# Performance work log

Measured on AMD Instinct MI355X. Metric: run time of the kernel, lower is better.

Reference implementation:

```python
import jax, jax.numpy as jnp
import numpy as np

D_MODEL = 1024
H = 16
DK = 64
DV = 64
D_OUT = 1024
SEQ = 1024
BATCH = 4


def setup_inputs() -> dict:
    key = jax.random.key(0)
    ks = jax.random.split(key, 11)
    s = 0.02
    return {
        "query": jax.random.normal(ks[0], (SEQ, BATCH, D_MODEL), jnp.float32),
        "key": jax.random.normal(ks[1], (SEQ, BATCH, D_MODEL), jnp.float32),
        "value": jax.random.normal(ks[2], (SEQ, BATCH, D_MODEL), jnp.float32),
        "Wq": jax.random.normal(ks[3], (D_MODEL, H * DK), jnp.float32) * s,
        "bq": jnp.zeros((H * DK,), jnp.float32),
        "Wk": jax.random.normal(ks[4], (D_MODEL, H * DK), jnp.float32) * s,
        "bk": jnp.zeros((H * DK,), jnp.float32),
        "Wv": jax.random.normal(ks[5], (D_MODEL, H * DV), jnp.float32) * s,
        "bv": jnp.zeros((H * DV,), jnp.float32),
        "Wo": jax.random.normal(ks[6], (H * DV, D_OUT), jnp.float32) * s,
        "bo": jnp.zeros((D_OUT,), jnp.float32),
    }


def reference(query, key, value, Wq, bq, Wk, bk, Wv, bv, Wo, bo):
    S, B, _ = query.shape
    # projections (seq-first layout, like the torch module)
    q = query @ Wq + bq            # (S, B, H*DK)
    k = key @ Wk + bk              # (S, B, H*DK)
    v = value @ Wv + bv            # (S, B, H*DV)
    # view + transpose(0, 2): (S, B, H, d) -> (H, B, S, d)
    q = jnp.transpose(q.reshape(S, B, H, DK), (2, 1, 0, 3))
    k = jnp.transpose(k.reshape(S, B, H, DK), (2, 1, 0, 3))
    v = jnp.transpose(v.reshape(S, B, H, DV), (2, 1, 0, 3))
    # scaled dot-product attention, full logits materialized as in the original
    logits = jnp.einsum("hbsd,hbtd->hbst", q, k) / jnp.sqrt(jnp.float32(DK))
    attn = jax.nn.softmax(logits, axis=-1)            # (H, B, S, S)
    ctx = jnp.einsum("hbst,hbtd->hbsd", attn, v)       # (H, B, S, DV)
    # transpose(0, 2) back and merge heads: (S, B, H*DV)
    ctx = jnp.transpose(ctx, (2, 1, 0, 3)).reshape(S, B, H * DV)
    out = ctx @ Wo + bo                               # (S, B, D_OUT)
    return (out, attn)
```

## Files before the change

### kernel.cpp

```cpp
#include <hip/hip_runtime.h>


typedef unsigned short u16;
typedef unsigned int u32;
typedef short short8v __attribute__((ext_vector_type(8)));
typedef short short4v __attribute__((ext_vector_type(4)));
typedef float f32x4 __attribute__((ext_vector_type(4)));

__device__ __forceinline__ u16 f2bf(float f) {
    u32 u = __builtin_bit_cast(u32, f);
    u += 0x7fffu + ((u >> 16) & 1u);
    return (u16)(u >> 16);
}

__device__ __forceinline__ f32x4 mfma_bf16(short8v a, short8v b, f32x4 c) {
    return __builtin_amdgcn_mfma_f32_16x16x32_bf16(a, b, c, 0, 0, 0);
}

__global__ __launch_bounds__(256) void cvt_transpose_w4(const float* __restrict__ W0,
                                                        const float* __restrict__ W1,
                                                        const float* __restrict__ W2,
                                                        const float* __restrict__ W3,
                                                        u16* __restrict__ T0, u16* __restrict__ T1,
                                                        u16* __restrict__ T2, u16* __restrict__ T3) {
    __shared__ u16 T[64][72];
    const float* W; u16* Wt;
    switch (blockIdx.y) {
        case 0: W = W0; Wt = T0; break;
        case 1: W = W1; Wt = T1; break;
        case 2: W = W2; Wt = T2; break;
        default: W = W3; Wt = T3; break;
    }
    const int n0 = (blockIdx.x & 15) << 6;
    const int k0 = (blockIdx.x >> 4) << 6;
    const int t = threadIdx.x;
    const int r = t >> 2;
    const int c = t & 3;
    const float4* src = reinterpret_cast<const float4*>(W + (size_t)(k0 + r) * 1024 + n0 + c * 16);
#pragma unroll
    for (int j = 0; j < 4; ++j) {
        float4 v = src[j];
        T[c * 16 + j * 4 + 0][r] = f2bf(v.x);
        T[c * 16 + j * 4 + 1][r] = f2bf(v.y);
        T[c * 16 + j * 4 + 2][r] = f2bf(v.z);
        T[c * 16 + j * 4 + 3][r] = f2bf(v.w);
    }
    __syncthreads();
    u16* dst = Wt + (size_t)(n0 + r) * 1024 + k0 + c * 16;
    *reinterpret_cast<short8v*>(dst)     = *reinterpret_cast<const short8v*>(&T[r][c * 16]);
    *reinterpret_cast<short8v*>(dst + 8) = *reinterpret_cast<const short8v*>(&T[r][c * 16 + 8]);
}

__global__ __launch_bounds__(256, 2) void gemm_qkv(const float* __restrict__ Aq,
                                                   const float* __restrict__ Ak,
                                                   const float* __restrict__ Av,
                                                   const u16* __restrict__ Wtq,
                                                   const u16* __restrict__ Wtk,
                                                   const u16* __restrict__ Wtv,
                                                   const float* __restrict__ bq,
                                                   const float* __restrict__ bk,
                                                   const float* __restrict__ bv,
                                                   u16* __restrict__ dq, u16* __restrict__ dk,
                                                   u16* __restrict__ dv) {
    __shared__ u16 As[128][72];
    __shared__ u16 Bs[128][72];
    const float* A; const u16* Wt; const float* bias; u16* dst;
    switch (blockIdx.z) {
        case 0: A = Aq; Wt = Wtq; bias = bq; dst = dq; break;
        case 1: A = Ak; Wt = Wtk; bias = bk; dst = dk; break;
        default: A = Av; Wt = Wtv; bias = bv; dst = dv; break;
    }
    const int m0 = blockIdx.y << 7;
    const int n0 = blockIdx.x << 7;
    const int t = threadIdx.x;
    const int lane = t & 63;
    const int w = t >> 6;
    const int wr = (w >> 1) << 6;
    const int wc = (w & 1) << 6;
    const int l15 = lane & 15, lg = lane >> 4;
    const int srow = t >> 1;
    const int sh = (t & 1) << 5;

    const float* Arow = A + (size_t)(m0 + srow) * 1024 + sh;
    const u16*   Brow = Wt + (size_t)(n0 + srow) * 1024 + sh;

    f32x4 acc[4][4] = {};
    float4 ra[8]; short8v rb[4];

    auto LOADR = [&](int kt) {
        const float4* ap = reinterpret_cast<const float4*>(Arow + kt * 64);
#pragma unroll
        for (int j = 0; j < 8; ++j) ra[j] = ap[j];
        const short8v* bp = reinterpret_cast<const short8v*>(Brow + kt * 64);
#pragma unroll
        for (int j = 0; j < 4; ++j) rb[j] = bp[j];
    };

    LOADR(0);
    for (int kt = 0; kt < 16; ++kt) {
        __syncthreads();
#pragma unroll
        for (int j = 0; j < 4; ++j) {
            float4 x = ra[2 * j], y = ra[2 * j + 1];
            short8v p;
            p[0] = (short)f2bf(x.x); p[1] = (short)f2bf(x.y);
            p[2] = (short)f2bf(x.z); p[3] = (short)f2bf(x.w);
            p[4] = (short)f2bf(y.x); p[5] = (short)f2bf(y.y);
            p[6] = (short)f2bf(y.z); p[7] = (short)f2bf(y.w);
            *reinterpret_cast<short8v*>(&As[srow][sh + j * 8]) = p;
            *reinterpret_cast<short8v*>(&Bs[srow][sh + j * 8]) = rb[j];
        }
        if (kt < 15) LOADR(kt + 1);
        __syncthreads();
#pragma unroll
        for (int kk = 0; kk < 2; ++kk) {
            short8v a[4], b[4];
#pragma unroll
            for (int m = 0; m < 4; ++m)
                a[m] = *reinterpret_cast<const short8v*>(&As[wr + m * 16 + l15][kk * 32 + lg * 8]);
#pragma unroll
            for (int n = 0; n < 4; ++n)
                b[n] = *reinterpret_cast<const short8v*>(&Bs[wc + n * 16 + l15][kk * 32 + lg * 8]);
#pragma unroll
            for (int m = 0; m < 4; ++m)
#pragma unroll
                for (int n = 0; n < 4; ++n)
                    acc[m][n] = mfma_bf16(a[m], b[n], acc[m][n]);
        }
    }

#pragma unroll
    for (int n = 0; n < 4; ++n) {
        const int c = n0 + wc + n * 16 + l15;
        const float bvv = bias[c];
        const int h = c >> 6, d = c & 63;
#pragma unroll
        for (int m = 0; m < 4; ++m) {
#pragma unroll
            for (int r = 0; r < 4; ++r) {
                const int mi = m0 + wr + m * 16 + lg * 4 + r;
                const int s = mi >> 2, bb = mi & 3;
                dst[(size_t)(((h << 2) + bb) << 16) + (s << 6) + d] = f2bf(acc[m][n][r] + bvv);
            }
        }
    }
}

__global__ __launch_bounds__(256) void transpose_v(const u16* __restrict__ vb,
                                                   u16* __restrict__ vtb) {
    __shared__ u16 T[64][72];
    const int hb = blockIdx.y;
    const int s0 = blockIdx.x << 6;
    const u16* src = vb + (size_t)hb * 65536;
    u16* dst = vtb + (size_t)hb * 65536;
    const int t = threadIdx.x;
    const int r = t >> 2;
    const int c = (t & 3) << 4;
    short8v v0 = *reinterpret_cast<const short8v*>(src + (size_t)(s0 + r) * 64 + c);
    short8v v1 = *reinterpret_cast<const short8v*>(src + (size_t)(s0 + r) * 64 + c + 8);
#pragma unroll
    for (int j = 0; j < 8; ++j) T[c + j][r] = (u16)v0[j];
#pragma unroll
    for (int j = 0; j < 8; ++j) T[c + 8 + j][r] = (u16)v1[j];
    __syncthreads();
    *reinterpret_cast<short8v*>(dst + (size_t)r * 1024 + s0 + c)     = *reinterpret_cast<const short8v*>(&T[r][c]);
    *reinterpret_cast<short8v*>(dst + (size_t)r * 1024 + s0 + c + 8) = *reinterpret_cast<const short8v*>(&T[r][c + 8]);
}

__global__ __launch_bounds__(512, 4) void attn_kernel(const u16* __restrict__ qb,
                                                      const u16* __restrict__ kb,
                                                      const u16* __restrict__ vtb,
                                                      float* __restrict__ attn_out,
                                                      u16* __restrict__ ctxb) {
    __shared__ float Sm[16 * 1024];
    char* Sb = (char*)Sm;
    const int hb = blockIdx.y;
    const int q0 = blockIdx.x << 4;
    const int h = hb >> 2, b = hb & 3;
    const int t = threadIdx.x;
    const int lane = t & 63, w = t >> 6;
    const int l15 = lane & 15, lg = lane >> 4;

    const u16* Q = qb + (size_t)hb * 65536;
    const u16* K = kb + (size_t)hb * 65536;
    const u16* VT = vtb + (size_t)hb * 65536;

    short8v aq[2];
#pragma unroll
    for (int kh = 0; kh < 2; ++kh)
        aq[kh] = *reinterpret_cast<const short8v*>(Q + (q0 + l15) * 64 + kh * 32 + lg * 8);

#pragma unroll
    for (int n = 0; n < 8; ++n) {
        const int tcol = w * 128 + n * 16 + l15;
        f32x4 acc = {};
#pragma unroll
        for (int kh = 0; kh < 2; ++kh) {
            short8v bk = *reinterpret_cast<const short8v*>(K + tcol * 64 + kh * 32 + lg * 8);
            acc = mfma_bf16(aq[kh], bk, acc);
        }
#pragma unroll
        for (int r = 0; r < 4; ++r) {
            const int row = lg * 4 + r;
            *(float*)(Sb + (row << 12) + (((tcol) << 2) ^ ((row & 7) << 4))) = acc[r] * 0.125f;
        }
    }
    __syncthreads();

#pragma unroll
    for (int rr = 0; rr < 2; ++rr) {
        const int r = w * 2 + rr;
        const int swz = (r & 7) << 4;
        f32x4 vv[4];
#pragma unroll
        for (int j = 0; j < 4; ++j)
            vv[j] = *(const f32x4*)(Sb + (r << 12) + (((lane * 4 + j * 256) << 2) ^ swz));
        float mx = -1e30f;
#pragma unroll
        for (int j = 0; j < 4; ++j)
#pragma unroll
            for (int i = 0; i < 4; ++i) mx = fmaxf(mx, vv[j][i]);
#pragma unroll
        for (int o = 1; o < 64; o <<= 1) mx = fmaxf(mx, __shfl_xor(mx, o, 64));
        float sum = 0.f;
#pragma unroll
        for (int j = 0; j < 4; ++j)
#pragma unroll
            for (int i = 0; i < 4; ++i) { vv[j][i] = __expf(vv[j][i] - mx); sum += vv[j][i]; }
#pragma unroll
        for (int o = 1; o < 64; o <<= 1) sum += __shfl_xor(sum, o, 64);
        const float inv = 1.0f / sum;
        float* grow = attn_out + (((size_t)(hb << 10) + q0 + r) << 10);
#pragma unroll
        for (int j = 0; j < 4; ++j) {
            f32x4 p = vv[j] * inv;
            *reinterpret_cast<f32x4*>(grow + lane * 4 + j * 256) = p;
            short4v pk;
            pk[0] = (short)f2bf(p[0]); pk[1] = (short)f2bf(p[1]);
            pk[2] = (short)f2bf(p[2]); pk[3] = (short)f2bf(p[3]);
            *(short4v*)(Sb + (r << 12) + (((lane * 4 + j * 256) << 1) ^ swz)) = pk;
        }
    }
    __syncthreads();

    f32x4 cacc[4] = {};
#pragma unroll
    for (int kt = 0; kt < 4; ++kt) {
        const int kcol = w * 128 + kt * 32 + lg * 8;
        short8v ap = *(const short8v*)(Sb + (l15 << 12) + (((kcol) << 1) ^ ((l15 & 7) << 4)));
#pragma unroll
        for (int n = 0; n < 4; ++n) {
            short8v bv = *reinterpret_cast<const short8v*>(VT + (size_t)(n * 16 + l15) * 1024 + kcol);
            cacc[n] = mfma_bf16(ap, bv, cacc[n]);
        }
    }
    __syncthreads();

    float* part = Sm;
#pragma unroll
    for (int n = 0; n < 4; ++n)
#pragma unroll
        for (int r = 0; r < 4; ++r)
            part[w * 1088 + (lg * 4 + r) * 68 + n * 16 + l15] = cacc[n][r];
    __syncthreads();
    if (t < 256) {
        const int rrow = t >> 4;
        const int c0 = (t & 15) << 2;
        f32x4 s = {};
#pragma unroll
        for (int ww = 0; ww < 8; ++ww)
            s += *reinterpret_cast<const f32x4*>(&part[ww * 1088 + rrow * 68 + c0]);
        short4v o;
        o[0] = (short)f2bf(s[0]); o[1] = (short)f2bf(s[1]);
        o[2] = (short)f2bf(s[2]); o[3] = (short)f2bf(s[3]);
        *reinterpret_cast<short4v*>(ctxb + (size_t)(((q0 + rrow) << 2) + b) * 1024 + h * 64 + c0) = o;
    }
}

__global__ __launch_bounds__(512, 2) void gemm_out(const u16* __restrict__ ctxb,
                                                   const u16* __restrict__ Wto,
                                                   const float* __restrict__ bo,
                                                   float* __restrict__ out) {
    __shared__ char LB[73728];
    const int m0 = blockIdx.y << 7;
    const int n0 = blockIdx.x << 7;
    const int t = threadIdx.x;
    const int lane = t & 63;
    const int w = t >> 6;
    const int grp = w >> 2;
    const int wl = w & 3;
    const int wr = (wl >> 1) << 6;
    const int wc = (wl & 1) << 6;
    const int l15 = lane & 15, lg = lane >> 4;
    const int tg = t & 255;
    const int srow = tg >> 1;
    const int sh = (tg & 1) << 5;

    u16 (*As)[72] = (u16(*)[72])(LB + grp * 36864);
    u16 (*Bs)[72] = (u16(*)[72])(LB + grp * 36864 + 18432);
    const int kb0 = grp << 9;

    const u16* Arow = ctxb + (size_t)(m0 + srow) * 1024 + kb0 + sh;
    const u16* Brow = Wto + (size_t)(n0 + srow) * 1024 + kb0 + sh;

    f32x4 acc[4][4] = {};
    short8v ra[4], rb[4];

    auto LOADR = [&](int s) {
        const short8v* ap = reinterpret_cast<const short8v*>(Arow + s * 64);
        const short8v* bp = reinterpret_cast<const short8v*>(Brow + s * 64);
#pragma unroll
        for (int j = 0; j < 4; ++j) { ra[j] = ap[j]; rb[j] = bp[j]; }
    };

    LOADR(0);
    for (int s = 0; s < 8; ++s) {
        __syncthreads();
#pragma unroll
        for (int j = 0; j < 4; ++j) {
            *reinterpret_cast<short8v*>(&As[srow][sh + j * 8]) = ra[j];
            *reinterpret_cast<short8v*>(&Bs[srow][sh + j * 8]) = rb[j];
        }
        if (s < 7) LOADR(s + 1);
        __syncthreads();
#pragma unroll
        for (int kk = 0; kk < 2; ++kk) {
            short8v a[4], b[4];
#pragma unroll
            for (int m = 0; m < 4; ++m)
                a[m] = *reinterpret_cast<const short8v*>(&As[wr + m * 16 + l15][kk * 32 + lg * 8]);
#pragma unroll
            for (int n = 0; n < 4; ++n)
                b[n] = *reinterpret_cast<const short8v*>(&Bs[wc + n * 16 + l15][kk * 32 + lg * 8]);
#pragma unroll
            for (int m = 0; m < 4; ++m)
#pragma unroll
                for (int n = 0; n < 4; ++n)
                    acc[m][n] = mfma_bf16(a[m], b[n], acc[m][n]);
        }
    }

    __syncthreads();
    float* part = (float*)LB;
    if (grp == 1) {
#pragma unroll
        for (int m = 0; m < 4; ++m)
#pragma unroll
            for (int n = 0; n < 4; ++n)
#pragma unroll
                for (int r = 0; r < 4; ++r)
                    part[(wr + m * 16 + lg * 4 + r) * 132 + wc + n * 16 + l15] = acc[m][n][r];
    }
    __syncthreads();
    if (grp == 0) {
#pragma unroll
        for (int n = 0; n < 4; ++n) {
            const int c = n0 + wc + n * 16 + l15;
            const float bvv = bo[c];
#pragma unroll
            for (int m = 0; m < 4; ++m)
#pragma unroll
                for (int r = 0; r < 4; ++r) {
                    const int mi = m0 + wr + m * 16 + lg * 4 + r;
                    out[(size_t)mi * 1024 + c] =
                        acc[m][n][r] + part[(wr + m * 16 + lg * 4 + r) * 132 + wc + n * 16 + l15] + bvv;
                }
        }
    }
}

extern "C" void kernel_launch(void* const* d_in, const int* in_sizes, int n_in,
                              void* d_out, int out_size, void* d_ws, size_t ws_size,
                              hipStream_t stream) {
    const float* query = (const float*)d_in[0];
    const float* key   = (const float*)d_in[1];
    const float* value = (const float*)d_in[2];
    const float* Wq = (const float*)d_in[3];
    const float* bq = (const float*)d_in[4];
    const float* Wk = (const float*)d_in[5];
    const float* bk = (const float*)d_in[6];
    const float* Wv = (const float*)d_in[7];
    const float* bv = (const float*)d_in[8];
    const float* Wo = (const float*)d_in[9];
    const float* bo = (const float*)d_in[10];

    char* ws = (char*)d_ws;
    u16* Wtq  = (u16*)(ws);
    u16* Wtk  = (u16*)(ws + ((size_t)2 << 20));
    u16* Wtv  = (u16*)(ws + ((size_t)4 << 20));
    u16* Wto  = (u16*)(ws + ((size_t)6 << 20));
    u16* qb   = (u16*)(ws + ((size_t)8 << 20));
    u16* kb   = (u16*)(ws + ((size_t)16 << 20));
    u16* vb   = (u16*)(ws + ((size_t)24 << 20));
    u16* vtb  = (u16*)(ws + ((size_t)32 << 20));
    u16* ctxb = (u16*)(ws + ((size_t)24 << 20));

    float* out  = (float*)d_out;
    float* attn = out + (size_t)4 * 1024 * 1024;

    cvt_transpose_w4<<<dim3(256, 4), 256, 0, stream>>>(Wq, Wk, Wv, Wo, Wtq, Wtk, Wtv, Wto);

    gemm_qkv<<<dim3(8, 32, 3), 256, 0, stream>>>(query, key, value, Wtq, Wtk, Wtv,
                                                 bq, bk, bv, qb, kb, vb);

    transpose_v<<<dim3(16, 64), 256, 0, stream>>>(vb, vtb);

    attn_kernel<<<dim3(64, 64), 512, 0, stream>>>(qb, kb, vtb, attn, ctxb);

    gemm_out<<<dim3(8, 32), 512, 0, stream>>>(ctxb, Wto, bo, out);
}
```

Before: 529.6 us.

## Pre-convert inputs to bf16 and stage GEMM tiles via direct global-to-LDS loads

A new kernel converts query/key/value to bf16 up front, writing 8-element chunks in a row-XOR swizzled order. The weight transpose and the attention context output use the same swizzle, so both GEMMs can fill unpadded LDS tiles with global_load_lds and read them without bank conflicts. gemm_qkv drops its register prefetch and in-kernel fp32 conversion, and its occupancy hint goes from 2 to 3. gemm_out is reshaped from a 512-thread split-K kernel with an LDS reduction to 256-thread 64x128 tiles over full K. The trade-offs are an extra pass over the inputs, extra workspace, and no register double-buffering, so each tile's load is exposed between barriers.

```diff
diff --git a/kernel.cpp b/kernel.cpp
--- a/kernel.cpp
+++ b/kernel.cpp
@@ -12,9 +12,37 @@
     u += 0x7fffu + ((u >> 16) & 1u);
     return (u16)(u >> 16);
 }
-
 __device__ __forceinline__ f32x4 mfma_bf16(short8v a, short8v b, f32x4 c) {
     return __builtin_amdgcn_mfma_f32_16x16x32_bf16(a, b, c, 0, 0, 0);
+}
+__device__ __forceinline__ void gload16(const void* g, void* l) {
+    __builtin_amdgcn_global_load_lds((const __attribute__((address_space(1))) u32*)g,
+                                     (__attribute__((address_space(3))) u32*)l, 16, 0, 0);
+}
+
+__global__ __launch_bounds__(256) void cvt_inputs(const float* __restrict__ X0,
+                                                  const float* __restrict__ X1,
+                                                  const float* __restrict__ X2,
+                                                  u16* __restrict__ Y0, u16* __restrict__ Y1,
+                                                  u16* __restrict__ Y2) {
+    const float* X; u16* Y;
+    switch (blockIdx.y) {
+        case 0: X = X0; Y = Y0; break;
+        case 1: X = X1; Y = Y1; break;
+        default: X = X2; Y = Y2; break;
+    }
+    const int tid = blockIdx.x * 256 + threadIdx.x;
+    const int row = tid >> 7;
+    const int c = tid & 127;
+    const float4* s4 = reinterpret_cast<const float4*>(X + (size_t)row * 1024 + c * 8);
+    float4 v0 = s4[0], v1 = s4[1];
+    short8v p;
+    p[0] = (short)f2bf(v0.x); p[1] = (short)f2bf(v0.y);
+    p[2] = (short)f2bf(v0.z); p[3] = (short)f2bf(v0.w);
+    p[4] = (short)f2bf(v1.x); p[5] = (short)f2bf(v1.y);
+    p[6] = (short)f2bf(v1.z); p[7] = (short)f2bf(v1.w);
+    const int dc = (c & ~7) | ((c ^ row) & 7);
+    *reinterpret_cast<short8v*>(Y + (size_t)row * 1024 + dc * 8) = p;
 }
 
 __global__ __launch_bounds__(256) void cvt_transpose_w4(const float* __restrict__ W0,
@@ -46,14 +74,17 @@
         T[c * 16 + j * 4 + 3][r] = f2bf(v.w);
     }
     __syncthreads();
-    u16* dst = Wt + (size_t)(n0 + r) * 1024 + k0 + c * 16;
-    *reinterpret_cast<short8v*>(dst)     = *reinterpret_cast<const short8v*>(&T[r][c * 16]);
-    *reinterpret_cast<short8v*>(dst + 8) = *reinterpret_cast<const short8v*>(&T[r][c * 16 + 8]);
-}
-
-__global__ __launch_bounds__(256, 2) void gemm_qkv(const float* __restrict__ Aq,
-                                                   const float* __restrict__ Ak,
-                                                   const float* __restrict__ Av,
+    const int s = r & 7;
+    const int p0 = (c << 1) ^ s;
+    const int p1 = ((c << 1) | 1) ^ s;
+    u16* base = Wt + (size_t)(n0 + r) * 1024 + k0;
+    *reinterpret_cast<short8v*>(base + p0 * 8) = *reinterpret_cast<const short8v*>(&T[r][c * 16]);
+    *reinterpret_cast<short8v*>(base + p1 * 8) = *reinterpret_cast<const short8v*>(&T[r][c * 16 + 8]);
+}
+
+__global__ __launch_bounds__(256, 3) void gemm_qkv(const u16* __restrict__ Abq,
+                                                   const u16* __restrict__ Abk,
+                                                   const u16* __restrict__ Abv,
                                                    const u16* __restrict__ Wtq,
                                                    const u16* __restrict__ Wtk,
                                                    const u16* __restrict__ Wtv,
@@ -62,13 +93,13 @@
                                                    const float* __restrict__ bv,
                                                    u16* __restrict__ dq, u16* __restrict__ dk,
                                                    u16* __restrict__ dv) {
-    __shared__ u16 As[128][72];
-    __shared__ u16 Bs[128][72];
-    const float* A; const u16* Wt; const float* bias; u16* dst;
+    __shared__ u16 As[128][64];
+    __shared__ u16 Bs[128][64];
+    const u16* Ab; const u16* Wt; const float* bias; u16* dst;
     switch (blockIdx.z) {
-        case 0: A = Aq; Wt = Wtq; bias = bq; dst = dq; break;
-        case 1: A = Ak; Wt = Wtk; bias = bk; dst = dk; break;
-        default: A = Av; Wt = Wtv; bias = bv; dst = dv; break;
+        case 0: Ab = Abq; Wt = Wtq; bias = bq; dst = dq; break;
+        case 1: Ab = Abk; Wt = Wtk; bias = bk; dst = dk; break;
+        default: Ab = Abv; Wt = Wtv; bias = bv; dst = dv; break;
     }
     const int m0 = blockIdx.y << 7;
     const int n0 = blockIdx.x << 7;
@@ -78,49 +109,34 @@
     const int wr = (w >> 1) << 6;
     const int wc = (w & 1) << 6;
     const int l15 = lane & 15, lg = lane >> 4;
-    const int srow = t >> 1;
-    const int sh = (t & 1) << 5;
-
-    const float* Arow = A + (size_t)(m0 + srow) * 1024 + sh;
-    const u16*   Brow = Wt + (size_t)(n0 + srow) * 1024 + sh;
+
+    const u16* ga = Ab + (size_t)(m0 + w * 32 + (lane >> 3)) * 1024 + (lane & 7) * 8;
+    const u16* gb = Wt + (size_t)(n0 + w * 32 + (lane >> 3)) * 1024 + (lane & 7) * 8;
 
     f32x4 acc[4][4] = {};
-    float4 ra[8]; short8v rb[4];
-
-    auto LOADR = [&](int kt) {
-        const float4* ap = reinterpret_cast<const float4*>(Arow + kt * 64);
-#pragma unroll
-        for (int j = 0; j < 8; ++j) ra[j] = ap[j];
-        const short8v* bp = reinterpret_cast<const short8v*>(Brow + kt * 64);
-#pragma unroll
-        for (int j = 0; j < 4; ++j) rb[j] = bp[j];
-    };
-
-    LOADR(0);
+
     for (int kt = 0; kt < 16; ++kt) {
-        __syncthreads();
+        const int k0 = kt << 6;
+        if (kt) __syncthreads();
 #pragma unroll
         for (int j = 0; j < 4; ++j) {
-            float4 x = ra[2 * j], y = ra[2 * j + 1];
-            short8v p;
-            p[0] = (short)f2bf(x.x); p[1] = (short)f2bf(x.y);
-            p[2] = (short)f2bf(x.z); p[3] = (short)f2bf(x.w);
-            p[4] = (short)f2bf(y.x); p[5] = (short)f2bf(y.y);
-            p[6] = (short)f2bf(y.z); p[7] = (short)f2bf(y.w);
-            *reinterpret_cast<short8v*>(&As[srow][sh + j * 8]) = p;
-            *reinterpret_cast<short8v*>(&Bs[srow][sh + j * 8]) = rb[j];
-        }
-        if (kt < 15) LOADR(kt + 1);
+            gload16(ga + j * 8 * 1024 + k0, &As[w * 32 + j * 8][0]);
+            gload16(gb + j * 8 * 1024 + k0, &Bs[w * 32 + j * 8][0]);
+        }
         __syncthreads();
 #pragma unroll
         for (int kk = 0; kk < 2; ++kk) {
             short8v a[4], b[4];
 #pragma unroll
-            for (int m = 0; m < 4; ++m)
-                a[m] = *reinterpret_cast<const short8v*>(&As[wr + m * 16 + l15][kk * 32 + lg * 8]);
-#pragma unroll
-            for (int n = 0; n < 4; ++n)
-                b[n] = *reinterpret_cast<const short8v*>(&Bs[wc + n * 16 + l15][kk * 32 + lg * 8]);
+            for (int m = 0; m < 4; ++m) {
+                const int row = wr + m * 16 + l15;
+                a[m] = *reinterpret_cast<const short8v*>(&As[row][(((kk << 2) | lg) ^ (row & 7)) << 3]);
+            }
+#pragma unroll
+            for (int n = 0; n < 4; ++n) {
+                const int row = wc + n * 16 + l15;
+                b[n] = *reinterpret_cast<const short8v*>(&Bs[row][(((kk << 2) | lg) ^ (row & 7)) << 3]);
+            }
 #pragma unroll
             for (int m = 0; m < 4; ++m)
 #pragma unroll
@@ -202,7 +218,7 @@
 #pragma unroll
         for (int r = 0; r < 4; ++r) {
             const int row = lg * 4 + r;
-            *(float*)(Sb + (row << 12) + (((tcol) << 2) ^ ((row & 7) << 4))) = acc[r] * 0.125f;
+            *(float*)(Sb + (row << 12) + ((tcol << 2) ^ ((row & 7) << 4))) = acc[r] * 0.125f;
         }
     }
     __syncthreads();
@@ -247,7 +263,7 @@
 #pragma unroll
     for (int kt = 0; kt < 4; ++kt) {
         const int kcol = w * 128 + kt * 32 + lg * 8;
-        short8v ap = *(const short8v*)(Sb + (l15 << 12) + (((kcol) << 1) ^ ((l15 & 7) << 4)));
+        short8v ap = *(const short8v*)(Sb + (l15 << 12) + ((kcol << 1) ^ ((l15 & 7) << 4)));
 #pragma unroll
         for (int n = 0; n < 4; ++n) {
             short8v bv = *reinterpret_cast<const short8v*>(VT + (size_t)(n * 16 + l15) * 1024 + kcol);
@@ -273,99 +289,74 @@
         short4v o;
         o[0] = (short)f2bf(s[0]); o[1] = (short)f2bf(s[1]);
         o[2] = (short)f2bf(s[2]); o[3] = (short)f2bf(s[3]);
-        *reinterpret_cast<short4v*>(ctxb + (size_t)(((q0 + rrow) << 2) + b) * 1024 + h * 64 + c0) = o;
-    }
-}
-
-__global__ __launch_bounds__(512, 2) void gemm_out(const u16* __restrict__ ctxb,
+        const int mi = ((q0 + rrow) << 2) + b;
+        const int off = h * 64 + (((c0 >> 3) ^ (mi & 7)) << 3) + (c0 & 7);
+        *reinterpret_cast<short4v*>(ctxb + (size_t)mi * 1024 + off) = o;
+    }
+}
+
+__global__ __launch_bounds__(256, 2) void gemm_out(const u16* __restrict__ ctxb,
                                                    const u16* __restrict__ Wto,
                                                    const float* __restrict__ bo,
                                                    float* __restrict__ out) {
-    __shared__ char LB[73728];
-    const int m0 = blockIdx.y << 7;
+    __shared__ u16 As[64][64];
+    __shared__ u16 Bs[128][64];
+    const int m0 = blockIdx.y << 6;
     const int n0 = blockIdx.x << 7;
     const int t = threadIdx.x;
     const int lane = t & 63;
     const int w = t >> 6;
-    const int grp = w >> 2;
-    const int wl = w & 3;
-    const int wr = (wl >> 1) << 6;
-    const int wc = (wl & 1) << 6;
+    const int wr = (w >> 1) << 5;
+    const int wc = (w & 1) << 6;
     const int l15 = lane & 15, lg = lane >> 4;
-    const int tg = t & 255;
-    const int srow = tg >> 1;
-    const int sh = (tg & 1) << 5;
-
-    u16 (*As)[72] = (u16(*)[72])(LB + grp * 36864);
-    u16 (*Bs)[72] = (u16(*)[72])(LB + grp * 36864 + 18432);
-    const int kb0 = grp << 9;
-
-    const u16* Arow = ctxb + (size_t)(m0 + srow) * 1024 + kb0 + sh;
-    const u16* Brow = Wto + (size_t)(n0 + srow) * 1024 + kb0 + sh;
-
-    f32x4 acc[4][4] = {};
-    short8v ra[4], rb[4];
-
-    auto LOADR = [&](int s) {
-        const short8v* ap = reinterpret_cast<const short8v*>(Arow + s * 64);
-        const short8v* bp = reinterpret_cast<const short8v*>(Brow + s * 64);
-#pragma unroll
-        for (int j = 0; j < 4; ++j) { ra[j] = ap[j]; rb[j] = bp[j]; }
-    };
-
-    LOADR(0);
-    for (int s = 0; s < 8; ++s) {
+
+    const u16* ga = ctxb + (size_t)(m0 + w * 16 + (lane >> 3)) * 1024 + (lane & 7) * 8;
+    const u16* gb = Wto + (size_t)(n0 + w * 32 + (lane >> 3)) * 1024 + (lane & 7) * 8;
+
+    f32x4 acc[2][4] = {};
+
+    for (int kt = 0; kt < 16; ++kt) {
+        const int k0 = kt << 6;
+        if (kt) __syncthreads();
+#pragma unroll
+        for (int j = 0; j < 2; ++j)
+            gload16(ga + j * 8 * 1024 + k0, &As[w * 16 + j * 8][0]);
+#pragma unroll
+        for (int j = 0; j < 4; ++j)
+            gload16(gb + j * 8 * 1024 + k0, &Bs[w * 32 + j * 8][0]);
         __syncthreads();
 #pragma unroll
-        for (int j = 0; j < 4; ++j) {
-            *reinterpret_cast<short8v*>(&As[srow][sh + j * 8]) = ra[j];
-            *reinterpret_cast<short8v*>(&Bs[srow][sh + j * 8]) = rb[j];
-        }
-        if (s < 7) LOADR(s + 1);
-        __syncthreads();
-#pragma unroll
         for (int kk = 0; kk < 2; ++kk) {
-            short8v a[4], b[4];
-#pragma unroll
-            for (int m = 0; m < 4; ++m)
-                a[m] = *reinterpret_cast<const short8v*>(&As[wr + m * 16 + l15][kk * 32 + lg * 8]);
-#pragma unroll
-            for (int n = 0; n < 4; ++n)
-                b[n] = *reinterpret_cast<const short8v*>(&Bs[wc + n * 16 + l15][kk * 32 + lg * 8]);
-#pragma unroll
-            for (int m = 0; m < 4; ++m)
+            short8v a[2], b[4];
+#pragma unroll
+            for (int m = 0; m < 2; ++m) {
+                const int row = wr + m * 16 + l15;
+                a[m] = *reinterpret_cast<const short8v*>(&As[row][(((kk << 2) | lg) ^ (row & 7)) << 3]);
+            }
+#pragma unroll
+            for (int n = 0; n < 4; ++n) {
+                const int row = wc + n * 16 + l15;
+                b[n] = *reinterpret_cast<const short8v*>(&Bs[row][(((kk << 2) | lg) ^ (row & 7)) << 3]);
+            }
+#pragma unroll
+            for (int m = 0; m < 2; ++m)
 #pragma unroll
                 for (int n = 0; n < 4; ++n)
                     acc[m][n] = mfma_bf16(a[m], b[n], acc[m][n]);
         }
     }
 
-    __syncthreads();
-    float* part = (float*)LB;
-    if (grp == 1) {
-#pragma unroll
-        for (int m = 0; m < 4; ++m)
-#pragma unroll
-            for (int n = 0; n < 4; ++n)
-#pragma unroll
-                for (int r = 0; r < 4; ++r)
-                    part[(wr + m * 16 + lg * 4 + r) * 132 + wc + n * 16 + l15] = acc[m][n][r];
-    }
-    __syncthreads();
-    if (grp == 0) {
-#pragma unroll
-        for (int n = 0; n < 4; ++n) {
-            const int c = n0 + wc + n * 16 + l15;
-            const float bvv = bo[c];
-#pragma unroll
-            for (int m = 0; m < 4; ++m)
-#pragma unroll
-                for (int r = 0; r < 4; ++r) {
-                    const int mi = m0 + wr + m * 16 + lg * 4 + r;
-                    out[(size_t)mi * 1024 + c] =
-                        acc[m][n][r] + part[(wr + m * 16 + lg * 4 + r) * 132 + wc + n * 16 + l15] + bvv;
-                }
-        }
+#pragma unroll
+    for (int n = 0; n < 4; ++n) {
+        const int c = n0 + wc + n * 16 + l15;
+        const float bvv = bo[c];
+#pragma unroll
+        for (int m = 0; m < 2; ++m)
+#pragma unroll
+            for (int r = 0; r < 4; ++r) {
+                const int mi = m0 + wr + m * 16 + lg * 4 + r;
+                out[(size_t)mi * 1024 + c] = acc[m][n][r] + bvv;
+            }
     }
 }
 
@@ -394,18 +385,22 @@
     u16* vb   = (u16*)(ws + ((size_t)24 << 20));
     u16* vtb  = (u16*)(ws + ((size_t)32 << 20));
     u16* ctxb = (u16*)(ws + ((size_t)24 << 20));
+    u16* Abq  = (u16*)(ws + ((size_t)40 << 20));
+    u16* Abk  = (u16*)(ws + ((size_t)48 << 20));
+    u16* Abv  = (u16*)(ws + ((size_t)56 << 20));
 
     float* out  = (float*)d_out;
     float* attn = out + (size_t)4 * 1024 * 1024;
 
     cvt_transpose_w4<<<dim3(256, 4), 256, 0, stream>>>(Wq, Wk, Wv, Wo, Wtq, Wtk, Wtv, Wto);
-
-    gemm_qkv<<<dim3(8, 32, 3), 256, 0, stream>>>(query, key, value, Wtq, Wtk, Wtv,
+    cvt_inputs<<<dim3(2048, 3), 256, 0, stream>>>(query, key, value, Abq, Abk, Abv);
+
+    gemm_qkv<<<dim3(8, 32, 3), 256, 0, stream>>>(Abq, Abk, Abv, Wtq, Wtk, Wtv,
                                                  bq, bk, bv, qb, kb, vb);
 
     transpose_v<<<dim3(16, 64), 256, 0, stream>>>(vb, vtb);
 
     attn_kernel<<<dim3(64, 64), 512, 0, stream>>>(qb, kb, vtb, attn, ctxb);
 
-    gemm_out<<<dim3(8, 32), 512, 0, stream>>>(ctxb, Wto, bo, out);
-}
+    gemm_out<<<dim3(8, 64), 256, 0, stream>>>(ctxb, Wto, bo, out);
+}
```

New measurement: 504.5 us. 1.05x faster.
